# Kernel tuning notes

Measured on AMD Instinct MI355X. Metric: run time of the kernel, lower is better.

Reference implementation:

```python
import jax, jax.numpy as jnp
import numpy as np

B = 64       # batch
D = 768      # embed dim
NH = 12      # heads
HD = 64      # head dim
P = 16       # patch size
IMG = 224
G = IMG // P # 14 patches per side
N = G * G    # 196 patch tokens
T = N + 1    # +CLS
M = 4 * D    # MLP hidden 3072
LE = 9       # early blocks (8 prefix + last_early)
LL = 3       # late ragged blocks
NC = 1000    # classes
TAU = 0.9    # ATS CDF keep threshold
SCALE = 1.0 / np.sqrt(float(HD))


def setup_inputs() -> dict:
    keys = iter(jax.random.split(jax.random.key(0), 48))
    def w(shape):
        return jax.random.normal(next(keys), shape, jnp.float32) * 0.02
    def layer_params(L, prefix, d):
        d[prefix + "ln1_g"] = jnp.ones((L, D)); d[prefix + "ln1_b"] = jnp.zeros((L, D))
        d[prefix + "qkv_w"] = w((L, D, 3 * D)); d[prefix + "qkv_b"] = jnp.zeros((L, 3 * D))
        d[prefix + "proj_w"] = w((L, D, D)); d[prefix + "proj_b"] = jnp.zeros((L, D))
        d[prefix + "ln2_g"] = jnp.ones((L, D)); d[prefix + "ln2_b"] = jnp.zeros((L, D))
        d[prefix + "fc1_w"] = w((L, D, M)); d[prefix + "fc1_b"] = jnp.zeros((L, M))
        d[prefix + "fc2_w"] = w((L, M, D)); d[prefix + "fc2_b"] = jnp.zeros((L, D))
    inp = {}
    inp["images"] = jax.random.normal(next(keys), (B, 3, IMG, IMG), jnp.float32)
    inp["patch_w"] = w((D, 3, P, P)); inp["patch_b"] = jnp.zeros((D,))
    inp["cls_token"] = w((1, 1, D)); inp["pos_embed"] = w((1, T, D))
    layer_params(LE, "e_", inp)
    layer_params(LL, "l_", inp)
    inp["norm_g"] = jnp.ones((D,)); inp["norm_b"] = jnp.zeros((D,))
    inp["head_w"] = w((D, NC)); inp["head_b"] = jnp.zeros((NC,))
    return inp


def _ln(x, g, b):
    m = x.mean(-1, keepdims=True)
    v = ((x - m) ** 2).mean(-1, keepdims=True)
    return (x - m) * jax.lax.rsqrt(v + 1e-6) * g + b


def _block(x, p, i, key_mask=None):
    # Pre-LN ViT block; returns (x, post-softmax attention weights).
    Bb, Tt, _ = x.shape
    y = _ln(x, p["ln1_g"][i], p["ln1_b"][i])
    qkv = (y @ p["qkv_w"][i] + p["qkv_b"][i]).reshape(Bb, Tt, 3, NH, HD)
    q, k, v = jnp.moveaxis(qkv, 2, 0)                      # each [B,T,H,HD]
    logits = jnp.einsum("bqhd,bkhd->bhqk", q, k) * SCALE
    if key_mask is not None:
        # ragged attention: dropped tokens never act as keys (== packed varlen attn)
        logits = jnp.where(key_mask[:, None, None, :], logits, -1e9)
    a = jax.nn.softmax(logits, axis=-1)
    o = jnp.einsum("bhqk,bkhd->bqhd", a, v).reshape(Bb, Tt, D)
    x = x + o @ p["proj_w"][i] + p["proj_b"][i]
    y = _ln(x, p["ln2_g"][i], p["ln2_b"][i])
    y = jax.nn.gelu(y @ p["fc1_w"][i] + p["fc1_b"][i], approximate=False)
    x = x + y @ p["fc2_w"][i] + p["fc2_b"][i]
    return x, a


def reference(images, patch_w, patch_b, cls_token, pos_embed,
              e_ln1_g, e_ln1_b, e_qkv_w, e_qkv_b, e_proj_w, e_proj_b,
              e_ln2_g, e_ln2_b, e_fc1_w, e_fc1_b, e_fc2_w, e_fc2_b,
              l_ln1_g, l_ln1_b, l_qkv_w, l_qkv_b, l_proj_w, l_proj_b,
              l_ln2_g, l_ln2_b, l_fc1_w, l_fc1_b, l_fc2_w, l_fc2_b,
              norm_g, norm_b, head_w, head_b):
    loc = dict(locals())
    e = {k[2:]: v for k, v in loc.items() if k.startswith("e_")}
    l = {k[2:]: v for k, v in loc.items() if k.startswith("l_")}

    # front: patch embed (stride-P conv as einsum) + CLS + pos
    xi = images.reshape(B, 3, G, P, G, P)
    tok = jnp.einsum("bchpwq,dcpq->bhwd", xi, patch_w).reshape(B, N, D) + patch_b
    x = jnp.concatenate([jnp.broadcast_to(cls_token, (B, 1, D)), tok], axis=1) + pos_embed

    # early prefix + last_early (capture attn)
    attn = None
    for i in range(LE):
        x, attn = _block(x, e, i)

    # ATS importance scores: CLS attention (head-avg) * token feature norm, normalized
    cls_attn = attn.mean(axis=1)[:, 0, 1:]                 # [B,N]
    raw = cls_attn * jnp.linalg.norm(x[:, 1:, :], axis=-1)
    s = raw / (raw.sum(-1, keepdims=True) + 1e-12)

    # CDF mask: keep highest-scoring tokens until cumulative importance reaches TAU
    order = jnp.argsort(-s, axis=-1)
    cdf = jnp.cumsum(jnp.take_along_axis(s, order, axis=-1), axis=-1)
    keep_sorted = (cdf <= TAU).at[:, 0].set(True)          # always keep best token
    mask = jnp.zeros((B, N), bool).at[jnp.arange(B)[:, None], order].set(keep_sorted)
    key_mask = jnp.concatenate([jnp.ones((B, 1), bool), mask], axis=1)  # CLS kept

    # ragged late blocks (masked attention == packed variable-length attention)
    for i in range(LL):
        x, _ = _block(x, l, i, key_mask)

    # back: gather CLS (position 0 == cu_seqlens offsets), norm, head
    cls = _ln(x[:, 0, :], norm_g, norm_b)
    return cls @ head_w + head_b
```

## Files before the change

kernel.cpp:

```cpp
#include <hip/hip_runtime.h>
#include <hip/hip_bf16.h>
#include <math.h>

typedef __attribute__((ext_vector_type(8))) short s16x8;
typedef __attribute__((ext_vector_type(4))) short s16x4;
typedef __attribute__((ext_vector_type(4))) float f32x4;

#define MP 12672
#define MREAL 12608
#define PROWS 12544
#define SCALE 0.125f

__device__ __forceinline__ float gelu_exact(float z) {
    return 0.5f * z * (1.f + erff(z * 0.7071067811865475f));
}

__global__ void zero_pad_rows(float* __restrict__ x) {
    int r = MREAL + blockIdx.x;
    x[(size_t)r * 768 + threadIdx.x] = 0.f;
}

__global__ void set_cls(const float* __restrict__ cls, const float* __restrict__ pos,
                        float* __restrict__ x) {
    int b = blockIdx.x, t = threadIdx.x;
    x[(size_t)b * 197 * 768 + t] = cls[t] + pos[t];
}

__global__ void cast_pw(const float* __restrict__ w, __hip_bfloat16* __restrict__ o, int n) {
    int i = blockIdx.x * 256 + threadIdx.x;
    if (i < n) o[i] = __float2bfloat16(w[i]);
}

__global__ void im2col_kernel(const float* __restrict__ img, __hip_bfloat16* __restrict__ P) {
    int row = blockIdx.x;
    int t = threadIdx.x;
    if (row >= PROWS) {
        for (int k = t; k < 768; k += 256) P[(size_t)row * 768 + k] = __float2bfloat16(0.f);
        return;
    }
    int b = row / 196, n = row % 196;
    int gh = n / 14, gw = n % 14;
    for (int k = t; k < 768; k += 256) {
        int c = k >> 8, rem = k & 255, p = rem >> 4, q = rem & 15;
        float v = img[((size_t)(b * 3 + c) * 224 + (gh * 16 + p)) * 224 + gw * 16 + q];
        P[(size_t)row * 768 + k] = __float2bfloat16(v);
    }
}

__global__ void transpose_cast(const float* __restrict__ W, __hip_bfloat16* __restrict__ Wt,
                               int K, int N) {
    __shared__ float tile[32][33];
    int n0 = blockIdx.x * 32, k0 = blockIdx.y * 32;
    int tx = threadIdx.x, ty = threadIdx.y;
    #pragma unroll
    for (int i = 0; i < 4; ++i)
        tile[ty + i * 8][tx] = W[(size_t)(k0 + ty + i * 8) * N + n0 + tx];
    __syncthreads();
    #pragma unroll
    for (int i = 0; i < 4; ++i)
        Wt[(size_t)(n0 + ty + i * 8) * K + k0 + tx] = __float2bfloat16(tile[tx][ty + i * 8]);
}

__global__ void ln_bf16(const float* __restrict__ x, const float* __restrict__ g,
                        const float* __restrict__ bia, __hip_bfloat16* __restrict__ y) {
    int row = blockIdx.x;
    const float* xr = x + (size_t)row * 768;
    __hip_bfloat16* yr = y + (size_t)row * 768;
    int t = threadIdx.x;
    float v[3];
    float s = 0.f, s2 = 0.f;
    #pragma unroll
    for (int i = 0; i < 3; ++i) { v[i] = xr[t + 256 * i]; s += v[i]; s2 += v[i] * v[i]; }
    __shared__ float r1[256], r2[256];
    r1[t] = s; r2[t] = s2; __syncthreads();
    for (int off = 128; off > 0; off >>= 1) {
        if (t < off) { r1[t] += r1[t + off]; r2[t] += r2[t + off]; }
        __syncthreads();
    }
    float mean = r1[0] * (1.f / 768.f);
    float var = r2[0] * (1.f / 768.f) - mean * mean;
    float rs = rsqrtf(var + 1e-6f);
    #pragma unroll
    for (int i = 0; i < 3; ++i) {
        int c = t + 256 * i;
        yr[c] = __float2bfloat16((v[i] - mean) * rs * g[c] + bia[c]);
    }
}

__global__ void ln_f32(const float* __restrict__ x, const float* __restrict__ g,
                       const float* __restrict__ bia, float* __restrict__ y,
                       size_t in_stride) {
    int row = blockIdx.x;
    const float* xr = x + (size_t)row * in_stride;
    float* yr = y + (size_t)row * 768;
    int t = threadIdx.x;
    float v[3];
    float s = 0.f, s2 = 0.f;
    #pragma unroll
    for (int i = 0; i < 3; ++i) { v[i] = xr[t + 256 * i]; s += v[i]; s2 += v[i] * v[i]; }
    __shared__ float r1[256], r2[256];
    r1[t] = s; r2[t] = s2; __syncthreads();
    for (int off = 128; off > 0; off >>= 1) {
        if (t < off) { r1[t] += r1[t + off]; r2[t] += r2[t + off]; }
        __syncthreads();
    }
    float mean = r1[0] * (1.f / 768.f);
    float var = r2[0] * (1.f / 768.f) - mean * mean;
    float rs = rsqrtf(var + 1e-6f);
    #pragma unroll
    for (int i = 0; i < 3; ++i) {
        int c = t + 256 * i;
        yr[c] = (v[i] - mean) * rs * g[c] + bia[c];
    }
}

template <int EPI>
__global__ __launch_bounds__(256)
void gemm_mfma(const __hip_bfloat16* __restrict__ A,
               const __hip_bfloat16* __restrict__ Bt,
               const float* __restrict__ bias,
               const float* res, float* Cf, __hip_bfloat16* Cb,
               const float* __restrict__ pos,
               int Nc, int K) {
    __shared__ short As[8192];
    __shared__ short Bs[8192];
    int tid = threadIdx.x;
    int lane = tid & 63, w = tid >> 6;
    int wr = w >> 1, wc = w & 1;
    int bm = blockIdx.y * 128, bn = blockIdx.x * 128;
    int l15 = lane & 15, lh = lane >> 4;
    f32x4 acc[4][4] = {};
    for (int k0 = 0; k0 < K; k0 += 64) {
        #pragma unroll
        for (int q = 0; q < 4; ++q) {
            int S = (w * 4 + q) * 64 + lane;
            int row = S >> 3;
            int c = (S & 7) ^ (row & 7);
            const __hip_bfloat16* sA = A + (size_t)(bm + row) * K + (k0 + c * 8);
            const __hip_bfloat16* sB = Bt + (size_t)(bn + row) * K + (k0 + c * 8);
            __builtin_amdgcn_global_load_lds(
                (const __attribute__((address_space(1))) void*)sA,
                (__attribute__((address_space(3))) void*)&As[(w * 4 + q) * 512], 16, 0, 0);
            __builtin_amdgcn_global_load_lds(
                (const __attribute__((address_space(1))) void*)sB,
                (__attribute__((address_space(3))) void*)&Bs[(w * 4 + q) * 512], 16, 0, 0);
        }
        __syncthreads();
        #pragma unroll
        for (int ks = 0; ks < 2; ++ks) {
            s16x8 av[4], bv[4];
            int c = ks * 4 + lh;
            #pragma unroll
            for (int i = 0; i < 4; ++i) {
                int ra = wr * 64 + i * 16 + l15;
                av[i] = *(const s16x8*)&As[(ra * 8 + (c ^ (ra & 7))) * 8];
                int rb = wc * 64 + i * 16 + l15;
                bv[i] = *(const s16x8*)&Bs[(rb * 8 + (c ^ (rb & 7))) * 8];
            }
            #pragma unroll
            for (int i = 0; i < 4; ++i)
                #pragma unroll
                for (int j = 0; j < 4; ++j)
                    acc[i][j] = __builtin_amdgcn_mfma_f32_16x16x32_bf16(av[i], bv[j], acc[i][j], 0, 0, 0);
        }
        __syncthreads();
    }
    #pragma unroll
    for (int i = 0; i < 4; ++i) {
        #pragma unroll
        for (int j = 0; j < 4; ++j) {
            int colg = bn + wc * 64 + j * 16 + l15;
            float bcol = bias[colg];
            #pragma unroll
            for (int r = 0; r < 4; ++r) {
                int rowg = bm + wr * 64 + i * 16 + lh * 4 + r;
                float v = acc[i][j][r] + bcol;
                if (EPI == 0) {
                    Cf[(size_t)rowg * Nc + colg] = v;
                } else if (EPI == 1) {
                    Cf[(size_t)rowg * Nc + colg] = v + res[(size_t)rowg * Nc + colg];
                } else if (EPI == 2) {
                    Cb[(size_t)rowg * Nc + colg] = __float2bfloat16(gelu_exact(v));
                } else if (EPI == 4) {
                    Cb[(size_t)rowg * Nc + colg] = __float2bfloat16(v);
                } else {
                    if (rowg < PROWS) {
                        int b = rowg / 196, n = rowg % 196;
                        Cf[((size_t)b * 197 + 1 + n) * 768 + colg] = v + pos[(size_t)(1 + n) * 768 + colg];
                    }
                }
            }
        }
    }
}

__global__ __launch_bounds__(256)
void attn_mfma(const __hip_bfloat16* __restrict__ qkvp, const int* __restrict__ key_mask,
               __hip_bfloat16* __restrict__ o, float* __restrict__ cls_row,
               int useMask, int saveCls) {
    int h = blockIdx.x, b = blockIdx.y;
    __shared__ short Kl[224 * 64];
    __shared__ short Vt[64 * 256];
    __shared__ short Pl[4][4096];
    __shared__ unsigned mword[7];
    const short* qkv = (const short*)qkvp;
    int t = threadIdx.x;

    if (t < 7) {
        unsigned wb = 0;
        for (int j = 0; j < 32; ++j) {
            int k = t * 32 + j;
            int bit = (k < 197) ? (useMask ? (key_mask[b * 197 + k] != 0) : 1) : 0;
            wb |= (unsigned)bit << j;
        }
        mword[t] = wb;
    }
    {
        int c = t & 7, kr0 = t >> 3;
        for (int it = 0; it < 7; ++it) {
            int krow = kr0 + it * 32;
            s16x8 v;
            if (krow < 197) {
                v = *(const s16x8*)(qkv + (size_t)(b * 197 + krow) * 2304 + 768 + h * 64 + c * 8);
            } else {
                #pragma unroll
                for (int j = 0; j < 8; ++j) v[j] = 0;
            }
            *(s16x8*)&Kl[(krow * 8 + (c ^ (krow & 7))) * 8] = v;
        }
    }
    {
        int d = t & 63, cb = t >> 6;
        for (int it = 0; it < 8; ++it) {
            int c = cb + it * 4;
            s16x8 v;
            #pragma unroll
            for (int j = 0; j < 8; ++j) {
                int k = c * 8 + j;
                v[j] = (k < 197) ? qkv[(size_t)(b * 197 + k) * 2304 + 1536 + h * 64 + d] : (short)0;
            }
            *(s16x8*)&Vt[(d * 32 + (c ^ (d & 7))) * 8] = v;
        }
    }
    __syncthreads();

    int w = t >> 6, lane = t & 63;
    int l15 = lane & 15, lh = lane >> 4;
    unsigned mw[7];
    #pragma unroll
    for (int i = 0; i < 7; ++i) mw[i] = mword[i];
    short* Pw = &Pl[w][0];

    for (int qf = w; qf < 13; qf += 4) {
        int qbase = qf * 16;
        int q = qbase + l15;
        const short* qptr = qkv + (size_t)(b * 197 + q) * 2304 + h * 64;
        s16x8 bq0 = *(const s16x8*)(qptr + lh * 8);
        s16x8 bq1 = *(const s16x8*)(qptr + 32 + lh * 8);

        f32x4 sacc[14];
        #pragma unroll
        for (int mf = 0; mf < 14; ++mf) sacc[mf] = (f32x4){0.f, 0.f, 0.f, 0.f};
        #pragma unroll
        for (int mf = 0; mf < 14; ++mf) {
            int row = mf * 16 + l15;
            s16x8 a0 = *(const s16x8*)&Kl[(row * 8 + (lh ^ (row & 7))) * 8];
            s16x8 a1 = *(const s16x8*)&Kl[(row * 8 + ((4 + lh) ^ (row & 7))) * 8];
            sacc[mf] = __builtin_amdgcn_mfma_f32_16x16x32_bf16(a0, bq0, sacc[mf], 0, 0, 0);
            sacc[mf] = __builtin_amdgcn_mfma_f32_16x16x32_bf16(a1, bq1, sacc[mf], 0, 0, 0);
        }
        float m = -1e30f;
        #pragma unroll
        for (int mf = 0; mf < 14; ++mf) {
            #pragma unroll
            for (int r = 0; r < 4; ++r) {
                int k = mf * 16 + lh * 4 + r;
                int keep = (mw[k >> 5] >> (k & 31)) & 1;
                float lg = keep ? sacc[mf][r] * SCALE : -1e30f;
                sacc[mf][r] = lg;
                m = fmaxf(m, lg);
            }
        }
        m = fmaxf(m, __shfl_xor(m, 16));
        m = fmaxf(m, __shfl_xor(m, 32));
        float sum = 0.f;
        #pragma unroll
        for (int mf = 0; mf < 14; ++mf) {
            #pragma unroll
            for (int r = 0; r < 4; ++r) {
                float p = expf(sacc[mf][r] - m);
                sum += p;
                sacc[mf][r] = p;
            }
        }
        sum += __shfl_xor(sum, 16);
        sum += __shfl_xor(sum, 32);
        float inv = 1.f / sum;
        if (saveCls && qf == 0 && l15 == 0) {
            #pragma unroll
            for (int mf = 0; mf < 14; ++mf)
                #pragma unroll
                for (int r = 0; r < 4; ++r) {
                    int k = mf * 16 + lh * 4 + r;
                    if (k < 197) cls_row[((size_t)b * 12 + h) * 197 + k] = sacc[mf][r] * inv;
                }
        }
        #pragma unroll
        for (int mf = 0; mf < 14; ++mf) {
            s16x4 pk;
            #pragma unroll
            for (int r = 0; r < 4; ++r) {
                __hip_bfloat16 hb = __float2bfloat16(sacc[mf][r] * inv);
                pk[r] = *(short*)&hb;
            }
            int slot = l15 * 32 + ((mf * 2 + (lh >> 1)) ^ (l15 & 7));
            *(s16x4*)&Pw[slot * 8 + (lh & 1) * 4] = pk;
        }
        f32x4 oacc[4];
        #pragma unroll
        for (int nf = 0; nf < 4; ++nf) oacc[nf] = (f32x4){0.f, 0.f, 0.f, 0.f};
        #pragma unroll
        for (int ks = 0; ks < 7; ++ks) {
            int c = ks * 4 + lh;
            s16x8 pa = *(const s16x8*)&Pw[(l15 * 32 + (c ^ (l15 & 7))) * 8];
            #pragma unroll
            for (int nf = 0; nf < 4; ++nf) {
                int d = nf * 16 + l15;
                s16x8 bv = *(const s16x8*)&Vt[(d * 32 + (c ^ (d & 7))) * 8];
                oacc[nf] = __builtin_amdgcn_mfma_f32_16x16x32_bf16(pa, bv, oacc[nf], 0, 0, 0);
            }
        }
        #pragma unroll
        for (int nf = 0; nf < 4; ++nf) {
            #pragma unroll
            for (int r = 0; r < 4; ++r) {
                int q2 = qbase + lh * 4 + r;
                if (q2 < 197)
                    o[(size_t)(b * 197 + q2) * 768 + h * 64 + nf * 16 + l15] =
                        __float2bfloat16(oacc[nf][r]);
            }
        }
    }
}

__global__ void cls_scores(const float* __restrict__ x, const float* __restrict__ cls_row,
                           float* __restrict__ raw) {
    int bn = blockIdx.x;
    int b = bn / 196, n = bn % 196;
    const float* xr = x + ((size_t)b * 197 + 1 + n) * 768;
    int t = threadIdx.x;
    float s2 = 0.f;
    for (int c = t; c < 768; c += 256) { float v = xr[c]; s2 += v * v; }
    __shared__ float r[256];
    r[t] = s2; __syncthreads();
    for (int off = 128; off > 0; off >>= 1) {
        if (t < off) r[t] += r[t + off];
        __syncthreads();
    }
    if (t == 0) {
        float ca = 0.f;
        for (int h = 0; h < 12; ++h) ca += cls_row[((size_t)b * 12 + h) * 197 + 1 + n];
        raw[bn] = (ca * (1.f / 12.f)) * sqrtf(r[0]);
    }
}

__global__ void ats_mask_kernel(const float* __restrict__ raw, int* __restrict__ key_mask) {
    int b = blockIdx.x, t = threadIdx.x;
    __shared__ float s[196];
    __shared__ float ssorted[196];
    __shared__ int keep[196];
    __shared__ float red[256];
    float v = (t < 196) ? raw[b * 196 + t] : 0.f;
    red[t] = v; __syncthreads();
    for (int off = 128; off > 0; off >>= 1) {
        if (t < off) red[t] += red[t + off];
        __syncthreads();
    }
    float total = red[0];
    if (t < 196) s[t] = v / (total + 1e-12f);
    __syncthreads();
    int rk = 0;
    if (t < 196) {
        float mys = s[t];
        for (int j = 0; j < 196; ++j) {
            float sj = s[j];
            rk += (sj > mys) || (sj == mys && j < t);
        }
        ssorted[rk] = mys;
    }
    __syncthreads();
    if (t == 0) {
        float c = 0.f;
        for (int k = 0; k < 196; ++k) {
            c += ssorted[k];
            keep[k] = (c <= 0.9f) || (k == 0);
        }
    }
    __syncthreads();
    if (t == 0) key_mask[b * 197] = 1;
    if (t < 196) key_mask[b * 197 + 1 + t] = keep[rk];
}

__global__ void gemm_head(const float* __restrict__ A, const float* __restrict__ W,
                          const float* __restrict__ bias, float* __restrict__ C,
                          int Mr, int Nc, int Kd) {
    __shared__ float As[16][65];
    __shared__ float Bs[16][65];
    int bm = blockIdx.y * 64, bn = blockIdx.x * 64;
    int tid = threadIdx.x;
    int tx = tid & 15, ty = tid >> 4;
    float acc[4][4] = {};
    for (int k0 = 0; k0 < Kd; k0 += 16) {
        for (int e = tid; e < 1024; e += 256) {
            int mm = e >> 4, k = e & 15;
            int row = bm + mm;
            As[k][mm] = (row < Mr) ? A[(size_t)row * Kd + k0 + k] : 0.f;
        }
        for (int e = tid; e < 1024; e += 256) {
            int k = e >> 6, n = e & 63;
            int col = bn + n;
            Bs[k][n] = (col < Nc) ? W[(size_t)(k0 + k) * Nc + col] : 0.f;
        }
        __syncthreads();
        #pragma unroll
        for (int kk = 0; kk < 16; ++kk) {
            float a0[4], b0[4];
            #pragma unroll
            for (int i = 0; i < 4; ++i) a0[i] = As[kk][ty * 4 + i];
            #pragma unroll
            for (int j = 0; j < 4; ++j) b0[j] = Bs[kk][tx * 4 + j];
            #pragma unroll
            for (int i = 0; i < 4; ++i)
                #pragma unroll
                for (int j = 0; j < 4; ++j) acc[i][j] += a0[i] * b0[j];
        }
        __syncthreads();
    }
    #pragma unroll
    for (int i = 0; i < 4; ++i) {
        int row = bm + ty * 4 + i;
        if (row >= Mr) continue;
        #pragma unroll
        for (int j = 0; j < 4; ++j) {
            int col = bn + tx * 4 + j;
            if (col >= Nc) continue;
            C[(size_t)row * Nc + col] = acc[i][j] + bias[col];
        }
    }
}

extern "C" void kernel_launch(void* const* d_in, const int* in_sizes, int n_in,
                              void* d_out, int out_size, void* d_ws, size_t ws_size,
                              hipStream_t stream) {
    const float* images  = (const float*)d_in[0];
    const float* patch_w = (const float*)d_in[1];
    const float* patch_b = (const float*)d_in[2];
    const float* cls_tok = (const float*)d_in[3];
    const float* pos_emb = (const float*)d_in[4];
    const float* e_p[12]; const float* l_p[12];
    for (int i = 0; i < 12; ++i) e_p[i] = (const float*)d_in[5 + i];
    for (int i = 0; i < 12; ++i) l_p[i] = (const float*)d_in[17 + i];
    const float* norm_g = (const float*)d_in[29];
    const float* norm_b = (const float*)d_in[30];
    const float* head_w = (const float*)d_in[31];
    const float* head_b = (const float*)d_in[32];
    float* out = (float*)d_out;

    float* ws = (float*)d_ws;
    size_t off = 0;
    float* x = ws + off; off += (size_t)MP * 768;
    __hip_bfloat16* ybf = (__hip_bfloat16*)(ws + off); off += (size_t)MP * 768 / 2;
    float* qh = ws + off; off += (size_t)MP * 3072;
    __hip_bfloat16* qbf = (__hip_bfloat16*)qh;
    __hip_bfloat16* P = (__hip_bfloat16*)qh;
    __hip_bfloat16* hbf = (__hip_bfloat16*)qh;
    __hip_bfloat16* wt = (__hip_bfloat16*)(ws + off); off += (size_t)7077888 / 2;
    __hip_bfloat16* pwb = (__hip_bfloat16*)(ws + off); off += (size_t)589824 / 2;
    float* clsrow = ws + off; off += (size_t)64 * 12 * 197;
    float* raw = ws + off; off += (size_t)64 * 196;
    float* clsln = ws + off; off += (size_t)64 * 768;
    int* kmask = (int*)(ws + off); off += (size_t)64 * 197;

    __hip_bfloat16* wt_qkv  = wt;
    __hip_bfloat16* wt_proj = wt_qkv + (size_t)2304 * 768;
    __hip_bfloat16* wt_fc1  = wt_proj + (size_t)768 * 768;
    __hip_bfloat16* wt_fc2  = wt_fc1 + (size_t)3072 * 768;

    zero_pad_rows<<<64, 768, 0, stream>>>(x);
    set_cls<<<64, 768, 0, stream>>>(cls_tok, pos_emb, x);
    cast_pw<<<2304, 256, 0, stream>>>(patch_w, pwb, 589824);
    im2col_kernel<<<MP, 256, 0, stream>>>(images, P);
    gemm_mfma<3><<<dim3(6, 99), 256, 0, stream>>>(P, pwb, patch_b, nullptr, x, nullptr,
                                                  pos_emb, 768, 768);

    for (int blk = 0; blk < 12; ++blk) {
        bool early = blk < 9;
        int i = early ? blk : blk - 9;
        const float* const* p = early ? e_p : l_p;
        const float* ln1g = p[0] + (size_t)i * 768;
        const float* ln1b = p[1] + (size_t)i * 768;
        const float* qkvw = p[2] + (size_t)i * 768 * 2304;
        const float* qkvb = p[3] + (size_t)i * 2304;
        const float* projw = p[4] + (size_t)i * 768 * 768;
        const float* projb = p[5] + (size_t)i * 768;
        const float* ln2g = p[6] + (size_t)i * 768;
        const float* ln2b = p[7] + (size_t)i * 768;
        const float* fc1w = p[8] + (size_t)i * 768 * 3072;
        const float* fc1b = p[9] + (size_t)i * 3072;
        const float* fc2w = p[10] + (size_t)i * 3072 * 768;
        const float* fc2b = p[11] + (size_t)i * 768;
        int useMask = early ? 0 : 1;
        int saveCls = (early && i == 8) ? 1 : 0;

        transpose_cast<<<dim3(72, 24), dim3(32, 8), 0, stream>>>(qkvw, wt_qkv, 768, 2304);
        transpose_cast<<<dim3(24, 24), dim3(32, 8), 0, stream>>>(projw, wt_proj, 768, 768);
        transpose_cast<<<dim3(96, 24), dim3(32, 8), 0, stream>>>(fc1w, wt_fc1, 768, 3072);
        transpose_cast<<<dim3(24, 96), dim3(32, 8), 0, stream>>>(fc2w, wt_fc2, 3072, 768);

        ln_bf16<<<MP, 256, 0, stream>>>(x, ln1g, ln1b, ybf);
        gemm_mfma<4><<<dim3(18, 99), 256, 0, stream>>>(ybf, wt_qkv, qkvb, nullptr, nullptr, qbf,
                                                       nullptr, 2304, 768);
        attn_mfma<<<dim3(12, 64), 256, 0, stream>>>(qbf, kmask, ybf, clsrow, useMask, saveCls);
        gemm_mfma<1><<<dim3(6, 99), 256, 0, stream>>>(ybf, wt_proj, projb, x, x, nullptr,
                                                      nullptr, 768, 768);
        ln_bf16<<<MP, 256, 0, stream>>>(x, ln2g, ln2b, ybf);
        gemm_mfma<2><<<dim3(24, 99), 256, 0, stream>>>(ybf, wt_fc1, fc1b, nullptr, nullptr, hbf,
                                                       nullptr, 3072, 768);
        gemm_mfma<1><<<dim3(6, 99), 256, 0, stream>>>(hbf, wt_fc2, fc2b, x, x, nullptr,
                                                      nullptr, 768, 3072);

        if (saveCls) {
            cls_scores<<<12544, 256, 0, stream>>>(x, clsrow, raw);
            ats_mask_kernel<<<64, 256, 0, stream>>>(raw, kmask);
        }
    }

    ln_f32<<<64, 256, 0, stream>>>(x, norm_g, norm_b, clsln, (size_t)197 * 768);
    gemm_head<<<dim3(16, 1), 256, 0, stream>>>(clsln, head_w, head_b, out, 64, 1000, 768);
}
```

Baseline: 5.217 ms.

## Merge weight transposes, swizzle GEMM blocks across XCDs, rewrite classifier head

Folds the four per-block weight transpose-cast launches into a single launch that dispatches on block index, cutting launch overhead. It remaps GEMM workgroup IDs so that consecutive tiles land on the same XCD, which is meant to improve L2 reuse on the multi-die GPU. It also replaces the tiled fp32 head GEMM with a transposed-activation kernel that uses one block per output column and reduces over K in shared memory, so the head runs on 1000 blocks instead of 16. The swizzle adds some index arithmetic per workgroup, and the new head kernel reads the head weights with strided accesses.

Result: faster. 4.894 ms, median of 2 (-6.2%).

```diff
diff --git a/kernel.cpp b/kernel.cpp
--- a/kernel.cpp
+++ b/kernel.cpp
@@ -47,10 +47,19 @@
     }
 }
 
-__global__ void transpose_cast(const float* __restrict__ W, __hip_bfloat16* __restrict__ Wt,
-                               int K, int N) {
+__global__ void transpose_cast_all(const float* __restrict__ qkvw,
+                                   const float* __restrict__ projw,
+                                   const float* __restrict__ fc1w,
+                                   const float* __restrict__ fc2w,
+                                   __hip_bfloat16* __restrict__ wt) {
     __shared__ float tile[32][33];
-    int n0 = blockIdx.x * 32, k0 = blockIdx.y * 32;
+    int bid = blockIdx.x;
+    const float* W; __hip_bfloat16* D; int K, N, tn;
+    if (bid < 1728) { W = qkvw; D = wt; K = 768; N = 2304; tn = 72; }
+    else if (bid < 2304) { bid -= 1728; W = projw; D = wt + 1769472; K = 768; N = 768; tn = 24; }
+    else if (bid < 4608) { bid -= 2304; W = fc1w; D = wt + 2359296; K = 768; N = 3072; tn = 96; }
+    else { bid -= 4608; W = fc2w; D = wt + 4718592; K = 3072; N = 768; tn = 24; }
+    int n0 = (bid % tn) * 32, k0 = (bid / tn) * 32;
     int tx = threadIdx.x, ty = threadIdx.y;
     #pragma unroll
     for (int i = 0; i < 4; ++i)
@@ -58,7 +67,7 @@
     __syncthreads();
     #pragma unroll
     for (int i = 0; i < 4; ++i)
-        Wt[(size_t)(n0 + ty + i * 8) * K + k0 + tx] = __float2bfloat16(tile[tx][ty + i * 8]);
+        D[(size_t)(n0 + ty + i * 8) * K + k0 + tx] = __float2bfloat16(tile[tx][ty + i * 8]);
 }
 
 __global__ void ln_bf16(const float* __restrict__ x, const float* __restrict__ g,
@@ -87,12 +96,10 @@
     }
 }
 
-__global__ void ln_f32(const float* __restrict__ x, const float* __restrict__ g,
-                       const float* __restrict__ bia, float* __restrict__ y,
-                       size_t in_stride) {
-    int row = blockIdx.x;
-    const float* xr = x + (size_t)row * in_stride;
-    float* yr = y + (size_t)row * 768;
+__global__ void ln_cls_t(const float* __restrict__ x, const float* __restrict__ g,
+                         const float* __restrict__ bia, float* __restrict__ At) {
+    int b = blockIdx.x;
+    const float* xr = x + (size_t)b * 197 * 768;
     int t = threadIdx.x;
     float v[3];
     float s = 0.f, s2 = 0.f;
@@ -110,7 +117,7 @@
     #pragma unroll
     for (int i = 0; i < 3; ++i) {
         int c = t + 256 * i;
-        yr[c] = (v[i] - mean) * rs * g[c] + bia[c];
+        At[(size_t)c * 64 + b] = (v[i] - mean) * rs * g[c] + bia[c];
     }
 }
 
@@ -127,7 +134,12 @@
     int tid = threadIdx.x;
     int lane = tid & 63, w = tid >> 6;
     int wr = w >> 1, wc = w & 1;
-    int bm = blockIdx.y * 128, bn = blockIdx.x * 128;
+    int nwg = gridDim.x * gridDim.y;
+    int bid = blockIdx.y * gridDim.x + blockIdx.x;
+    int xcd = bid & 7, idx = bid >> 3;
+    int qq = nwg >> 3, rr = nwg & 7;
+    int swz = (xcd < rr ? xcd * (qq + 1) : rr * (qq + 1) + (xcd - rr) * qq) + idx;
+    int bm = (swz / gridDim.x) * 128, bn = (swz % gridDim.x) * 128;
     int l15 = lane & 15, lh = lane >> 4;
     f32x4 acc[4][4] = {};
     for (int k0 = 0; k0 < K; k0 += 64) {
@@ -401,52 +413,21 @@
     if (t < 196) key_mask[b * 197 + 1 + t] = keep[rk];
 }
 
-__global__ void gemm_head(const float* __restrict__ A, const float* __restrict__ W,
-                          const float* __restrict__ bias, float* __restrict__ C,
-                          int Mr, int Nc, int Kd) {
-    __shared__ float As[16][65];
-    __shared__ float Bs[16][65];
-    int bm = blockIdx.y * 64, bn = blockIdx.x * 64;
-    int tid = threadIdx.x;
-    int tx = tid & 15, ty = tid >> 4;
-    float acc[4][4] = {};
-    for (int k0 = 0; k0 < Kd; k0 += 16) {
-        for (int e = tid; e < 1024; e += 256) {
-            int mm = e >> 4, k = e & 15;
-            int row = bm + mm;
-            As[k][mm] = (row < Mr) ? A[(size_t)row * Kd + k0 + k] : 0.f;
-        }
-        for (int e = tid; e < 1024; e += 256) {
-            int k = e >> 6, n = e & 63;
-            int col = bn + n;
-            Bs[k][n] = (col < Nc) ? W[(size_t)(k0 + k) * Nc + col] : 0.f;
-        }
-        __syncthreads();
-        #pragma unroll
-        for (int kk = 0; kk < 16; ++kk) {
-            float a0[4], b0[4];
-            #pragma unroll
-            for (int i = 0; i < 4; ++i) a0[i] = As[kk][ty * 4 + i];
-            #pragma unroll
-            for (int j = 0; j < 4; ++j) b0[j] = Bs[kk][tx * 4 + j];
-            #pragma unroll
-            for (int i = 0; i < 4; ++i)
-                #pragma unroll
-                for (int j = 0; j < 4; ++j) acc[i][j] += a0[i] * b0[j];
-        }
-        __syncthreads();
-    }
-    #pragma unroll
-    for (int i = 0; i < 4; ++i) {
-        int row = bm + ty * 4 + i;
-        if (row >= Mr) continue;
-        #pragma unroll
-        for (int j = 0; j < 4; ++j) {
-            int col = bn + tx * 4 + j;
-            if (col >= Nc) continue;
-            C[(size_t)row * Nc + col] = acc[i][j] + bias[col];
-        }
-    }
+__global__ void gemm_head_t(const float* __restrict__ At, const float* __restrict__ W,
+                            const float* __restrict__ bias, float* __restrict__ out) {
+    int col = blockIdx.x;
+    int t = threadIdx.x;
+    int row = t & 63, part = t >> 6;
+    float acc = 0.f;
+    for (int i = 0; i < 192; ++i) {
+        int k = part * 192 + i;
+        acc += At[(size_t)k * 64 + row] * W[(size_t)k * 1000 + col];
+    }
+    __shared__ float red[256];
+    red[t] = acc; __syncthreads();
+    if (part == 0)
+        out[(size_t)row * 1000 + col] = red[row] + red[64 + row] + red[128 + row] + red[192 + row]
+                                        + bias[col];
 }
 
 extern "C" void kernel_launch(void* const* d_in, const int* in_sizes, int n_in,
@@ -478,7 +459,7 @@
     __hip_bfloat16* pwb = (__hip_bfloat16*)(ws + off); off += (size_t)589824 / 2;
     float* clsrow = ws + off; off += (size_t)64 * 12 * 197;
     float* raw = ws + off; off += (size_t)64 * 196;
-    float* clsln = ws + off; off += (size_t)64 * 768;
+    float* At = ws + off; off += (size_t)768 * 64;
     int* kmask = (int*)(ws + off); off += (size_t)64 * 197;
 
     __hip_bfloat16* wt_qkv  = wt;
@@ -512,10 +493,7 @@
         int useMask = early ? 0 : 1;
         int saveCls = (early && i == 8) ? 1 : 0;
 
-        transpose_cast<<<dim3(72, 24), dim3(32, 8), 0, stream>>>(qkvw, wt_qkv, 768, 2304);
-        transpose_cast<<<dim3(24, 24), dim3(32, 8), 0, stream>>>(projw, wt_proj, 768, 768);
-        transpose_cast<<<dim3(96, 24), dim3(32, 8), 0, stream>>>(fc1w, wt_fc1, 768, 3072);
-        transpose_cast<<<dim3(24, 96), dim3(32, 8), 0, stream>>>(fc2w, wt_fc2, 3072, 768);
+        transpose_cast_all<<<6912, dim3(32, 8), 0, stream>>>(qkvw, projw, fc1w, fc2w, wt);
 
         ln_bf16<<<MP, 256, 0, stream>>>(x, ln1g, ln1b, ybf);
         gemm_mfma<4><<<dim3(18, 99), 256, 0, stream>>>(ybf, wt_qkv, qkvb, nullptr, nullptr, qbf,
@@ -535,6 +513,6 @@
         }
     }
 
-    ln_f32<<<64, 256, 0, stream>>>(x, norm_g, norm_b, clsln, (size_t)197 * 768);
-    gemm_head<<<dim3(16, 1), 256, 0, stream>>>(clsln, head_w, head_b, out, 64, 1000, 768);
-}
+    ln_cls_t<<<64, 256, 0, stream>>>(x, norm_g, norm_b, At);
+    gemm_head_t<<<1000, 256, 0, stream>>>(At, head_w, head_b, out);
+}
```
